# Performance work log

Measured on AMD Instinct MI355X. Metric: run time of the kernel, lower is better.

The kernel has to match this reference:

```python
import jax, jax.numpy as jnp
import numpy as np

N_NODES = 100000
N_EDGES = 1600000
D = 128
N_LAYERS = 3  # GIN num_layers = n_layers + 1 with n_layers = 2
BN_EPS = 1e-5


def _batchnorm(x, gamma, beta):
    # Training-mode BatchNorm1d over the node axis (biased variance, as torch uses
    # for normalization).
    mean = jnp.mean(x, axis=0)
    var = jnp.mean((x - mean) ** 2, axis=0)
    return (x - mean) * jax.lax.rsqrt(var + BN_EPS) * gamma + beta


def setup_inputs() -> dict:
    key = jax.random.key(0)
    ks = jax.random.split(key, 5)
    features = jax.random.normal(ks[0], (N_NODES, D), dtype=jnp.float32)
    W = jax.random.normal(ks[1], (N_LAYERS, D, D), dtype=jnp.float32) * 0.05
    b = jnp.zeros((N_LAYERS, D), dtype=jnp.float32)
    eps = jnp.zeros((N_LAYERS,), dtype=jnp.float32)  # learn_eps init 0
    bn1_gamma = jnp.ones((N_LAYERS, D), dtype=jnp.float32)
    bn1_beta = jnp.zeros((N_LAYERS, D), dtype=jnp.float32)
    bn2_gamma = jnp.ones((N_LAYERS, D), dtype=jnp.float32)
    bn2_beta = jnp.zeros((N_LAYERS, D), dtype=jnp.float32)
    src = jax.random.randint(ks[2], (N_EDGES,), 0, N_NODES, dtype=jnp.int64 if jax.config.jax_enable_x64 else jnp.int32)
    dst = jax.random.randint(ks[3], (N_EDGES,), 0, N_NODES, dtype=jnp.int64 if jax.config.jax_enable_x64 else jnp.int32)
    return {
        'features': features, 'W': W, 'b': b, 'eps': eps,
        'bn1_gamma': bn1_gamma, 'bn1_beta': bn1_beta,
        'bn2_gamma': bn2_gamma, 'bn2_beta': bn2_beta,
        'src': src, 'dst': dst,
    }


def reference(features, W, b, eps, bn1_gamma, bn1_beta, bn2_gamma, bn2_beta, src, dst):
    n = features.shape[0]
    h = features
    hidden_rep = [h]
    for i in range(N_LAYERS):
        # GINConv, 'sum' aggregation: (1+eps)*h_v + sum_{u->v} h_u
        agg = jax.ops.segment_sum(h[src], dst, num_segments=n)
        z = (1.0 + eps[i]) * h + agg
        # ApplyNodeFunc: Linear (num_mlp_layers=1) -> BN -> ReLU
        z = z @ W[i] + b[i]
        z = jax.nn.relu(_batchnorm(z, bn1_gamma[i], bn1_beta[i]))
        # GIN.forward: outer BN -> ReLU
        z = jax.nn.relu(_batchnorm(z, bn2_gamma[i], bn2_beta[i]))
        h = z
        hidden_rep.append(h)
    # torch.stack(hidden_rep) -> [n_layers+2, N, D]
    return jnp.stack(hidden_rep, axis=0)
```

## Files before the change

### kernel.cpp

```cpp
#include <hip/hip_runtime.h>
#include <hip/hip_bf16.h>

#define DD 128

typedef __attribute__((ext_vector_type(8))) short bfrag8;
typedef __attribute__((ext_vector_type(4))) float f32x4;

__device__ __forceinline__ float bf16lo(unsigned int u) {
    union { unsigned int i; float f; } c; c.i = u << 16; return c.f;
}
__device__ __forceinline__ float bf16hi(unsigned int u) {
    union { unsigned int i; float f; } c; c.i = u & 0xffff0000u; return c.f;
}
__device__ __forceinline__ unsigned short f2bf(float f) {
    union { float f; unsigned int i; } c; c.f = f;
    unsigned int x = c.i;
    unsigned int r = (x + 0x7fffu + ((x >> 16) & 1u)) >> 16;
    return (unsigned short)r;
}

__global__ void k_hist(const int* __restrict__ dst, int* __restrict__ deg, int E) {
    int i = blockIdx.x * blockDim.x + threadIdx.x;
    if (i < E) atomicAdd(&deg[dst[i]], 1);
}

__global__ void k_scan1(const int* __restrict__ deg, int* __restrict__ partials, int Nn) {
    __shared__ int s[1024];
    int i = blockIdx.x * 1024 + threadIdx.x;
    s[threadIdx.x] = (i < Nn) ? deg[i] : 0;
    __syncthreads();
    for (int off = 512; off > 0; off >>= 1) {
        if (threadIdx.x < off) s[threadIdx.x] += s[threadIdx.x + off];
        __syncthreads();
    }
    if (threadIdx.x == 0) partials[blockIdx.x] = s[0];
}

__global__ void k_scan2(const int* __restrict__ partials, int* __restrict__ pscan, int nb) {
    if (threadIdx.x == 0) {
        int acc = 0;
        for (int i = 0; i < nb; i++) { pscan[i] = acc; acc += partials[i]; }
    }
}

__global__ void k_scan3(const int* __restrict__ deg, const int* __restrict__ pscan,
                        int* __restrict__ row_start, int Nn, int E) {
    __shared__ int s[1024];
    int i = blockIdx.x * 1024 + threadIdx.x;
    int v = (i < Nn) ? deg[i] : 0;
    s[threadIdx.x] = v;
    __syncthreads();
    for (int off = 1; off < 1024; off <<= 1) {
        int t = (threadIdx.x >= off) ? s[threadIdx.x - off] : 0;
        __syncthreads();
        s[threadIdx.x] += t;
        __syncthreads();
    }
    if (i < Nn) row_start[i] = pscan[blockIdx.x] + s[threadIdx.x] - v;
    if (blockIdx.x == 0 && threadIdx.x == 0) row_start[Nn] = E;
}

__global__ void k_scatter(const int* __restrict__ src, const int* __restrict__ dst,
                          const int* __restrict__ row_start, int* __restrict__ cursor,
                          int* __restrict__ csr, int E) {
    int i = blockIdx.x * blockDim.x + threadIdx.x;
    if (i < E) {
        int d = dst[i];
        int pos = row_start[d] + atomicAdd(&cursor[d], 1);
        csr[pos] = src[i];
    }
}

__global__ void k_cvt_feat(const float* __restrict__ f, float* __restrict__ out0,
                           unsigned int* __restrict__ hb, int total4) {
    int i = blockIdx.x * blockDim.x + threadIdx.x;
    if (i >= total4) return;
    float4 v = ((const float4*)f)[i];
    ((float4*)out0)[i] = v;
    unsigned int lo = (unsigned int)f2bf(v.x) | ((unsigned int)f2bf(v.y) << 16);
    unsigned int hi = (unsigned int)f2bf(v.z) | ((unsigned int)f2bf(v.w) << 16);
    ((uint2*)hb)[i] = make_uint2(lo, hi);
}

__global__ void k_cvtW(const float* __restrict__ W, unsigned short* __restrict__ Wt, int total) {
    int i = blockIdx.x * blockDim.x + threadIdx.x;
    if (i >= total) return;
    int l = i >> 14;
    int r = i & 16383;
    int k = r >> 7, n = r & 127;
    Wt[(l << 14) + n * 128 + k] = f2bf(W[i]);
}

__global__ void k_gather(const unsigned int* __restrict__ hb, const int* __restrict__ row_start,
                         const int* __restrict__ csr, const float* __restrict__ eps, int layer,
                         unsigned int* __restrict__ zb, int Nn) {
    int wv = threadIdx.x >> 6, lane = threadIdx.x & 63;
    int v = blockIdx.x * 4 + wv;
    if (v >= Nn) return;
    float e1 = 1.0f + eps[layer];
    unsigned int hs = hb[v * 64 + lane];
    float ax = e1 * bf16lo(hs);
    float ay = e1 * bf16hi(hs);
    int beg = row_start[v], end = row_start[v + 1];
    int e = beg;
    for (; e + 3 < end; e += 4) {
        int u0 = csr[e], u1 = csr[e + 1], u2 = csr[e + 2], u3 = csr[e + 3];
        unsigned int h0 = hb[u0 * 64 + lane];
        unsigned int h1 = hb[u1 * 64 + lane];
        unsigned int h2 = hb[u2 * 64 + lane];
        unsigned int h3 = hb[u3 * 64 + lane];
        ax += bf16lo(h0) + bf16lo(h1) + bf16lo(h2) + bf16lo(h3);
        ay += bf16hi(h0) + bf16hi(h1) + bf16hi(h2) + bf16hi(h3);
    }
    for (; e < end; e++) {
        unsigned int hu = hb[csr[e] * 64 + lane];
        ax += bf16lo(hu); ay += bf16hi(hu);
    }
    zb[v * 64 + lane] = (unsigned int)f2bf(ax) | ((unsigned int)f2bf(ay) << 16);
}

__launch_bounds__(256)
__global__ void k_gemm(const unsigned short* __restrict__ zb, const unsigned short* __restrict__ Wt,
                       const float* __restrict__ bias, int layer, float* __restrict__ y,
                       float* __restrict__ s1sum, float* __restrict__ s1sq, int Nn) {
    __shared__ unsigned short Al[64 * 136];
    __shared__ unsigned short Bl[128 * 136];
    int tid = threadIdx.x;
    int m0 = blockIdx.x * 64;
    const unsigned short* Wl = Wt + (layer << 14);
    #pragma unroll
    for (int p = 0; p < 8; p++) {
        int slot = p * 256 + tid;
        int n = slot >> 4, c = slot & 15;
        *(uint4*)&Bl[n * 136 + c * 8] = *(const uint4*)&Wl[n * 128 + c * 8];
    }
    #pragma unroll
    for (int p = 0; p < 4; p++) {
        int slot = p * 256 + tid;
        int r = slot >> 4, c = slot & 15;
        int grow = m0 + r;
        uint4 val = make_uint4(0, 0, 0, 0);
        if (grow < Nn) val = *(const uint4*)&zb[(size_t)grow * 128 + c * 8];
        *(uint4*)&Al[r * 136 + c * 8] = val;
    }
    __syncthreads();

    int lane = tid & 63, wv = tid >> 6;
    int tcol = lane & 15, quad = lane >> 4;
    f32x4 acc[4][2];
    #pragma unroll
    for (int a = 0; a < 4; a++)
        #pragma unroll
        for (int b2 = 0; b2 < 2; b2++) acc[a][b2] = (f32x4){0.f, 0.f, 0.f, 0.f};

    #pragma unroll
    for (int kk = 0; kk < 128; kk += 32) {
        int kb = kk + quad * 8;
        bfrag8 af[4], bf[2];
        #pragma unroll
        for (int mt = 0; mt < 4; mt++)
            af[mt] = *(const bfrag8*)&Al[(16 * mt + tcol) * 136 + kb];
        #pragma unroll
        for (int nt = 0; nt < 2; nt++)
            bf[nt] = *(const bfrag8*)&Bl[(32 * wv + 16 * nt + tcol) * 136 + kb];
        #pragma unroll
        for (int mt = 0; mt < 4; mt++)
            #pragma unroll
            for (int nt = 0; nt < 2; nt++)
                acc[mt][nt] = __builtin_amdgcn_mfma_f32_16x16x32_bf16(af[mt], bf[nt], acc[mt][nt], 0, 0, 0);
    }

    #pragma unroll
    for (int nt = 0; nt < 2; nt++) {
        int col = 32 * wv + 16 * nt + tcol;
        float bcol = bias[layer * 128 + col];
        float psum = 0.f, psq = 0.f;
        #pragma unroll
        for (int mt = 0; mt < 4; mt++) {
            #pragma unroll
            for (int r = 0; r < 4; r++) {
                int row = m0 + 16 * mt + quad * 4 + r;
                float val = acc[mt][nt][r] + bcol;
                if (row < Nn) {
                    y[(size_t)row * 128 + col] = val;
                    psum += val;
                    psq += val * val;
                }
            }
        }
        psum += __shfl_xor(psum, 16); psq += __shfl_xor(psq, 16);
        psum += __shfl_xor(psum, 32); psq += __shfl_xor(psq, 32);
        if (lane < 16) {
            atomicAdd(&s1sum[col], psum);
            atomicAdd(&s1sq[col], psq);
        }
    }
}

__global__ void k_fin(float* __restrict__ sum, float* __restrict__ sq,
                      const float* __restrict__ gamma, const float* __restrict__ beta, int layer,
                      float* __restrict__ sc, float* __restrict__ sh, float invN) {
    int c = threadIdx.x;
    float m = sum[c] * invN;
    float var = sq[c] * invN - m * m;
    float rstd = rsqrtf(var + 1e-5f);
    float s = gamma[layer * 128 + c] * rstd;
    sc[c] = s;
    sh[c] = beta[layer * 128 + c] - m * s;
    sum[c] = 0.f;
    sq[c] = 0.f;
}

__global__ void k_stats2(const float* __restrict__ y, const float* __restrict__ s1,
                         const float* __restrict__ sh1, float* __restrict__ s2sum,
                         float* __restrict__ s2sq, int Nn) {
    int c = threadIdx.x & 127;
    int r0 = blockIdx.x * 2 + (threadIdx.x >> 7);
    float sc = s1[c], sh = sh1[c];
    float sum = 0.f, sq = 0.f;
    int stride = gridDim.x * 2;
    for (int r = r0; r < Nn; r += stride) {
        float t = fmaxf(y[(size_t)r * 128 + c] * sc + sh, 0.f);
        sum += t;
        sq += t * t;
    }
    atomicAdd(&s2sum[c], sum);
    atomicAdd(&s2sq[c], sq);
}

__global__ void k_apply(float* __restrict__ y, const float* __restrict__ s1,
                        const float* __restrict__ sh1, const float* __restrict__ s2,
                        const float* __restrict__ sh2, unsigned int* __restrict__ hb, int total4) {
    int i = blockIdx.x * blockDim.x + threadIdx.x;
    if (i >= total4) return;
    int c = (i * 4) & 127;
    float4 v = ((float4*)y)[i];
    float t0 = fmaxf(v.x * s1[c] + sh1[c], 0.f);
    float t1 = fmaxf(v.y * s1[c + 1] + sh1[c + 1], 0.f);
    float t2 = fmaxf(v.z * s1[c + 2] + sh1[c + 2], 0.f);
    float t3 = fmaxf(v.w * s1[c + 3] + sh1[c + 3], 0.f);
    float o0 = fmaxf(t0 * s2[c] + sh2[c], 0.f);
    float o1 = fmaxf(t1 * s2[c + 1] + sh2[c + 1], 0.f);
    float o2 = fmaxf(t2 * s2[c + 2] + sh2[c + 2], 0.f);
    float o3 = fmaxf(t3 * s2[c + 3] + sh2[c + 3], 0.f);
    ((float4*)y)[i] = make_float4(o0, o1, o2, o3);
    unsigned int lo = (unsigned int)f2bf(o0) | ((unsigned int)f2bf(o1) << 16);
    unsigned int hi = (unsigned int)f2bf(o2) | ((unsigned int)f2bf(o3) << 16);
    ((uint2*)hb)[i] = make_uint2(lo, hi);
}

extern "C" void kernel_launch(void* const* d_in, const int* in_sizes, int n_in,
                              void* d_out, int out_size, void* d_ws, size_t ws_size,
                              hipStream_t stream) {
    const float* features = (const float*)d_in[0];
    const float* W        = (const float*)d_in[1];
    const float* bias     = (const float*)d_in[2];
    const float* eps      = (const float*)d_in[3];
    const float* g1       = (const float*)d_in[4];
    const float* b1       = (const float*)d_in[5];
    const float* g2       = (const float*)d_in[6];
    const float* b2       = (const float*)d_in[7];
    const int*   src      = (const int*)d_in[8];
    const int*   dst      = (const int*)d_in[9];

    const int Nn = in_sizes[0] / DD;
    const int E  = in_sizes[8];
    const int L  = 3;
    float* out = (float*)d_out;

    char* w = (char*)d_ws;
    auto alloc = [&](size_t bytes) -> char* {
        char* p = w;
        w += (bytes + 255) & ~(size_t)255;
        return p;
    };
    int* deg       = (int*)alloc((size_t)Nn * 4);
    int* cursor    = (int*)alloc((size_t)Nn * 4);
    int* row_start = (int*)alloc((size_t)(Nn + 1) * 4);
    int* partials  = (int*)alloc(1024);
    int* pscan     = (int*)alloc(1024);
    int* csr       = (int*)alloc((size_t)E * 4);
    unsigned int* hb = (unsigned int*)alloc((size_t)Nn * 64 * 4);
    unsigned int* zb = (unsigned int*)alloc((size_t)Nn * 64 * 4);
    unsigned short* Wt = (unsigned short*)alloc((size_t)3 * 128 * 128 * 2);
    float* s1sum = (float*)alloc(512);
    float* s1sq  = (float*)alloc(512);
    float* s2sum = (float*)alloc(512);
    float* s2sq  = (float*)alloc(512);
    float* s1    = (float*)alloc(512);
    float* sh1   = (float*)alloc(512);
    float* s2    = (float*)alloc(512);
    float* sh2   = (float*)alloc(512);

    hipMemsetAsync(deg, 0, (size_t)Nn * 4, stream);
    hipMemsetAsync(cursor, 0, (size_t)Nn * 4, stream);
    hipMemsetAsync(s1sum, 0, 4 * 512, stream);

    const int nb = (Nn + 1023) / 1024;
    k_hist<<<(E + 255) / 256, 256, 0, stream>>>(dst, deg, E);
    k_scan1<<<nb, 1024, 0, stream>>>(deg, partials, Nn);
    k_scan2<<<1, 64, 0, stream>>>(partials, pscan, nb);
    k_scan3<<<nb, 1024, 0, stream>>>(deg, pscan, row_start, Nn, E);
    k_scatter<<<(E + 255) / 256, 256, 0, stream>>>(src, dst, row_start, cursor, csr, E);

    const int total4 = Nn * DD / 4;
    k_cvt_feat<<<(total4 + 255) / 256, 256, 0, stream>>>(features, out, hb, total4);
    k_cvtW<<<(3 * 128 * 128 + 255) / 256, 256, 0, stream>>>(W, Wt, 3 * 128 * 128);

    const float invN = 1.0f / (float)Nn;
    for (int l = 0; l < L; l++) {
        float* y = out + (size_t)(l + 1) * Nn * DD;
        k_gather<<<(Nn + 3) / 4, 256, 0, stream>>>(hb, row_start, csr, eps, l, zb, Nn);
        k_gemm<<<(Nn + 63) / 64, 256, 0, stream>>>((const unsigned short*)zb, Wt, bias, l, y,
                                                   s1sum, s1sq, Nn);
        k_fin<<<1, 128, 0, stream>>>(s1sum, s1sq, g1, b1, l, s1, sh1, invN);
        k_stats2<<<512, 256, 0, stream>>>(y, s1, sh1, s2sum, s2sq, Nn);
        k_fin<<<1, 128, 0, stream>>>(s2sum, s2sq, g2, b2, l, s2, sh2, invN);
        k_apply<<<(total4 + 255) / 256, 256, 0, stream>>>(y, s1, sh1, s2, sh2, hb, total4);
    }
}
```

Measured before the change: 991.3 us.

## Fuse setup kernels, fold BN finalize into stats/apply, unroll gather by eight

Merges histogram, feature conversion and weight conversion into one grid-stride setup kernel, and collapses the three-kernel scan into two with vectorised 4-per-thread loads. The BN finalize kernels are removed: stats2 and apply now compute scale and shift in shared memory, and stats2 reduces per block before doing global atomics. The gather loop is unrolled to eight neighbours for more loads in flight. The GEMM now writes to a scratch buffer instead of the output, and per-layer stats buffers are zeroed by a single memset. This cuts launch count and global atomic traffic, at the cost of redundant per-block finalize work and extra workspace memory.

```diff
diff --git a/kernel.cpp b/kernel.cpp
--- a/kernel.cpp
+++ b/kernel.cpp
@@ -19,45 +19,88 @@
     return (unsigned short)r;
 }
 
-__global__ void k_hist(const int* __restrict__ dst, int* __restrict__ deg, int E) {
-    int i = blockIdx.x * blockDim.x + threadIdx.x;
-    if (i < E) atomicAdd(&deg[dst[i]], 1);
+__global__ void k_setup(const int* __restrict__ dst, int* __restrict__ deg, int E,
+                        const float* __restrict__ features, float* __restrict__ out0,
+                        unsigned int* __restrict__ hb, int total4,
+                        const float* __restrict__ W, unsigned short* __restrict__ Wt) {
+    int gtid = blockIdx.x * blockDim.x + threadIdx.x;
+    int gsz = gridDim.x * blockDim.x;
+    for (int i = gtid; i < E; i += gsz) atomicAdd(&deg[dst[i]], 1);
+    for (int i = gtid; i < total4; i += gsz) {
+        float4 v = ((const float4*)features)[i];
+        ((float4*)out0)[i] = v;
+        unsigned int lo = (unsigned int)f2bf(v.x) | ((unsigned int)f2bf(v.y) << 16);
+        unsigned int hi = (unsigned int)f2bf(v.z) | ((unsigned int)f2bf(v.w) << 16);
+        ((uint2*)hb)[i] = make_uint2(lo, hi);
+    }
+    for (int i = gtid; i < 3 * 128 * 128; i += gsz) {
+        int l = i >> 14, r = i & 16383, k = r >> 7, n = r & 127;
+        Wt[(l << 14) + n * 128 + k] = f2bf(W[i]);
+    }
 }
 
 __global__ void k_scan1(const int* __restrict__ deg, int* __restrict__ partials, int Nn) {
-    __shared__ int s[1024];
-    int i = blockIdx.x * 1024 + threadIdx.x;
-    s[threadIdx.x] = (i < Nn) ? deg[i] : 0;
-    __syncthreads();
-    for (int off = 512; off > 0; off >>= 1) {
-        if (threadIdx.x < off) s[threadIdx.x] += s[threadIdx.x + off];
-        __syncthreads();
-    }
-    if (threadIdx.x == 0) partials[blockIdx.x] = s[0];
-}
-
-__global__ void k_scan2(const int* __restrict__ partials, int* __restrict__ pscan, int nb) {
-    if (threadIdx.x == 0) {
-        int acc = 0;
-        for (int i = 0; i < nb; i++) { pscan[i] = acc; acc += partials[i]; }
-    }
-}
-
-__global__ void k_scan3(const int* __restrict__ deg, const int* __restrict__ pscan,
-                        int* __restrict__ row_start, int Nn, int E) {
-    __shared__ int s[1024];
-    int i = blockIdx.x * 1024 + threadIdx.x;
-    int v = (i < Nn) ? deg[i] : 0;
-    s[threadIdx.x] = v;
-    __syncthreads();
-    for (int off = 1; off < 1024; off <<= 1) {
-        int t = (threadIdx.x >= off) ? s[threadIdx.x - off] : 0;
-        __syncthreads();
-        s[threadIdx.x] += t;
-        __syncthreads();
-    }
-    if (i < Nn) row_start[i] = pscan[blockIdx.x] + s[threadIdx.x] - v;
-    if (blockIdx.x == 0 && threadIdx.x == 0) row_start[Nn] = E;
+    __shared__ int sm[256];
+    int tid = threadIdx.x;
+    int base = (blockIdx.x << 10) + 4 * tid;
+    int s = 0;
+    if (base + 3 < Nn) {
+        int4 v = *(const int4*)&deg[base];
+        s = v.x + v.y + v.z + v.w;
+    } else {
+        for (int j = 0; j < 4; j++) if (base + j < Nn) s += deg[base + j];
+    }
+    sm[tid] = s;
+    __syncthreads();
+    for (int off = 128; off > 0; off >>= 1) {
+        if (tid < off) sm[tid] += sm[tid + off];
+        __syncthreads();
+    }
+    if (tid == 0) partials[blockIdx.x] = sm[0];
+}
+
+__global__ void k_scan3(const int* __restrict__ deg, const int* __restrict__ partials,
+                        int* __restrict__ row_start, int Nn, int E, int nchunk) {
+    __shared__ int sp[256];
+    __shared__ int sm[256];
+    int tid = threadIdx.x, c = blockIdx.x;
+    int p = (tid < nchunk) ? partials[tid] : 0;
+    sp[tid] = p;
+    __syncthreads();
+    for (int off = 1; off < 256; off <<= 1) {
+        int t = (tid >= off) ? sp[tid - off] : 0;
+        __syncthreads();
+        sp[tid] += t;
+        __syncthreads();
+    }
+    int chunkpref = (c == 0) ? 0 : sp[c - 1];
+
+    int base = (c << 10) + 4 * tid;
+    int d0 = 0, d1 = 0, d2 = 0, d3 = 0;
+    if (base + 3 < Nn) {
+        int4 v = *(const int4*)&deg[base];
+        d0 = v.x; d1 = v.y; d2 = v.z; d3 = v.w;
+    } else {
+        if (base + 0 < Nn) d0 = deg[base + 0];
+        if (base + 1 < Nn) d1 = deg[base + 1];
+        if (base + 2 < Nn) d2 = deg[base + 2];
+        if (base + 3 < Nn) d3 = deg[base + 3];
+    }
+    int ts = d0 + d1 + d2 + d3;
+    sm[tid] = ts;
+    __syncthreads();
+    for (int off = 1; off < 256; off <<= 1) {
+        int t = (tid >= off) ? sm[tid - off] : 0;
+        __syncthreads();
+        sm[tid] += t;
+        __syncthreads();
+    }
+    int run = chunkpref + sm[tid] - ts;
+    if (base + 0 < Nn) row_start[base + 0] = run; run += d0;
+    if (base + 1 < Nn) row_start[base + 1] = run; run += d1;
+    if (base + 2 < Nn) row_start[base + 2] = run; run += d2;
+    if (base + 3 < Nn) row_start[base + 3] = run;
+    if (c == 0 && tid == 0) row_start[Nn] = E;
 }
 
 __global__ void k_scatter(const int* __restrict__ src, const int* __restrict__ dst,
@@ -71,26 +114,6 @@
     }
 }
 
-__global__ void k_cvt_feat(const float* __restrict__ f, float* __restrict__ out0,
-                           unsigned int* __restrict__ hb, int total4) {
-    int i = blockIdx.x * blockDim.x + threadIdx.x;
-    if (i >= total4) return;
-    float4 v = ((const float4*)f)[i];
-    ((float4*)out0)[i] = v;
-    unsigned int lo = (unsigned int)f2bf(v.x) | ((unsigned int)f2bf(v.y) << 16);
-    unsigned int hi = (unsigned int)f2bf(v.z) | ((unsigned int)f2bf(v.w) << 16);
-    ((uint2*)hb)[i] = make_uint2(lo, hi);
-}
-
-__global__ void k_cvtW(const float* __restrict__ W, unsigned short* __restrict__ Wt, int total) {
-    int i = blockIdx.x * blockDim.x + threadIdx.x;
-    if (i >= total) return;
-    int l = i >> 14;
-    int r = i & 16383;
-    int k = r >> 7, n = r & 127;
-    Wt[(l << 14) + n * 128 + k] = f2bf(W[i]);
-}
-
 __global__ void k_gather(const unsigned int* __restrict__ hb, const int* __restrict__ row_start,
                          const int* __restrict__ csr, const float* __restrict__ eps, int layer,
                          unsigned int* __restrict__ zb, int Nn) {
@@ -98,31 +121,38 @@
     int v = blockIdx.x * 4 + wv;
     if (v >= Nn) return;
     float e1 = 1.0f + eps[layer];
-    unsigned int hs = hb[v * 64 + lane];
+    unsigned int hs = hb[(size_t)v * 64 + lane];
     float ax = e1 * bf16lo(hs);
     float ay = e1 * bf16hi(hs);
     int beg = row_start[v], end = row_start[v + 1];
     int e = beg;
-    for (; e + 3 < end; e += 4) {
+    for (; e + 7 < end; e += 8) {
         int u0 = csr[e], u1 = csr[e + 1], u2 = csr[e + 2], u3 = csr[e + 3];
-        unsigned int h0 = hb[u0 * 64 + lane];
-        unsigned int h1 = hb[u1 * 64 + lane];
-        unsigned int h2 = hb[u2 * 64 + lane];
-        unsigned int h3 = hb[u3 * 64 + lane];
-        ax += bf16lo(h0) + bf16lo(h1) + bf16lo(h2) + bf16lo(h3);
-        ay += bf16hi(h0) + bf16hi(h1) + bf16hi(h2) + bf16hi(h3);
+        int u4 = csr[e + 4], u5 = csr[e + 5], u6 = csr[e + 6], u7 = csr[e + 7];
+        unsigned int h0 = hb[(size_t)u0 * 64 + lane];
+        unsigned int h1 = hb[(size_t)u1 * 64 + lane];
+        unsigned int h2 = hb[(size_t)u2 * 64 + lane];
+        unsigned int h3 = hb[(size_t)u3 * 64 + lane];
+        unsigned int h4 = hb[(size_t)u4 * 64 + lane];
+        unsigned int h5 = hb[(size_t)u5 * 64 + lane];
+        unsigned int h6 = hb[(size_t)u6 * 64 + lane];
+        unsigned int h7 = hb[(size_t)u7 * 64 + lane];
+        ax += bf16lo(h0) + bf16lo(h1) + bf16lo(h2) + bf16lo(h3)
+            + bf16lo(h4) + bf16lo(h5) + bf16lo(h6) + bf16lo(h7);
+        ay += bf16hi(h0) + bf16hi(h1) + bf16hi(h2) + bf16hi(h3)
+            + bf16hi(h4) + bf16hi(h5) + bf16hi(h6) + bf16hi(h7);
     }
     for (; e < end; e++) {
-        unsigned int hu = hb[csr[e] * 64 + lane];
+        unsigned int hu = hb[(size_t)csr[e] * 64 + lane];
         ax += bf16lo(hu); ay += bf16hi(hu);
     }
-    zb[v * 64 + lane] = (unsigned int)f2bf(ax) | ((unsigned int)f2bf(ay) << 16);
+    zb[(size_t)v * 64 + lane] = (unsigned int)f2bf(ax) | ((unsigned int)f2bf(ay) << 16);
 }
 
 __launch_bounds__(256)
 __global__ void k_gemm(const unsigned short* __restrict__ zb, const unsigned short* __restrict__ Wt,
                        const float* __restrict__ bias, int layer, float* __restrict__ y,
-                       float* __restrict__ s1sum, float* __restrict__ s1sq, int Nn) {
+                       float* __restrict__ stl, int Nn) {
     __shared__ unsigned short Al[64 * 136];
     __shared__ unsigned short Bl[128 * 136];
     int tid = threadIdx.x;
@@ -191,62 +221,114 @@
         psum += __shfl_xor(psum, 16); psq += __shfl_xor(psq, 16);
         psum += __shfl_xor(psum, 32); psq += __shfl_xor(psq, 32);
         if (lane < 16) {
-            atomicAdd(&s1sum[col], psum);
-            atomicAdd(&s1sq[col], psq);
+            atomicAdd(&stl[col], psum);
+            atomicAdd(&stl[128 + col], psq);
         }
     }
 }
 
-__global__ void k_fin(float* __restrict__ sum, float* __restrict__ sq,
-                      const float* __restrict__ gamma, const float* __restrict__ beta, int layer,
-                      float* __restrict__ sc, float* __restrict__ sh, float invN) {
-    int c = threadIdx.x;
-    float m = sum[c] * invN;
-    float var = sq[c] * invN - m * m;
-    float rstd = rsqrtf(var + 1e-5f);
-    float s = gamma[layer * 128 + c] * rstd;
-    sc[c] = s;
-    sh[c] = beta[layer * 128 + c] - m * s;
-    sum[c] = 0.f;
-    sq[c] = 0.f;
-}
-
-__global__ void k_stats2(const float* __restrict__ y, const float* __restrict__ s1,
-                         const float* __restrict__ sh1, float* __restrict__ s2sum,
-                         float* __restrict__ s2sq, int Nn) {
-    int c = threadIdx.x & 127;
-    int r0 = blockIdx.x * 2 + (threadIdx.x >> 7);
-    float sc = s1[c], sh = sh1[c];
-    float sum = 0.f, sq = 0.f;
-    int stride = gridDim.x * 2;
-    for (int r = r0; r < Nn; r += stride) {
-        float t = fmaxf(y[(size_t)r * 128 + c] * sc + sh, 0.f);
-        sum += t;
-        sq += t * t;
-    }
-    atomicAdd(&s2sum[c], sum);
-    atomicAdd(&s2sq[c], sq);
-}
-
-__global__ void k_apply(float* __restrict__ y, const float* __restrict__ s1,
-                        const float* __restrict__ sh1, const float* __restrict__ s2,
-                        const float* __restrict__ sh2, unsigned int* __restrict__ hb, int total4) {
-    int i = blockIdx.x * blockDim.x + threadIdx.x;
-    if (i >= total4) return;
-    int c = (i * 4) & 127;
-    float4 v = ((float4*)y)[i];
-    float t0 = fmaxf(v.x * s1[c] + sh1[c], 0.f);
-    float t1 = fmaxf(v.y * s1[c + 1] + sh1[c + 1], 0.f);
-    float t2 = fmaxf(v.z * s1[c + 2] + sh1[c + 2], 0.f);
-    float t3 = fmaxf(v.w * s1[c + 3] + sh1[c + 3], 0.f);
-    float o0 = fmaxf(t0 * s2[c] + sh2[c], 0.f);
-    float o1 = fmaxf(t1 * s2[c + 1] + sh2[c + 1], 0.f);
-    float o2 = fmaxf(t2 * s2[c + 2] + sh2[c + 2], 0.f);
-    float o3 = fmaxf(t3 * s2[c + 3] + sh2[c + 3], 0.f);
-    ((float4*)y)[i] = make_float4(o0, o1, o2, o3);
-    unsigned int lo = (unsigned int)f2bf(o0) | ((unsigned int)f2bf(o1) << 16);
-    unsigned int hi = (unsigned int)f2bf(o2) | ((unsigned int)f2bf(o3) << 16);
-    ((uint2*)hb)[i] = make_uint2(lo, hi);
+__launch_bounds__(256)
+__global__ void k_stats2(const float* __restrict__ y, float* __restrict__ stl,
+                         const float* __restrict__ g1, const float* __restrict__ b1,
+                         int layer, int total4, float invN) {
+    __shared__ float red[512];
+    int tid = threadIdx.x;
+    if (tid < 128) {
+        float m = stl[tid] * invN;
+        float var = stl[128 + tid] * invN - m * m;
+        float rstd = rsqrtf(var + 1e-5f);
+        float s = g1[layer * 128 + tid] * rstd;
+        red[tid] = s;
+        red[128 + tid] = b1[layer * 128 + tid] - m * s;
+        red[256 + tid] = 0.f;
+        red[384 + tid] = 0.f;
+    }
+    __syncthreads();
+    int lane = tid & 63;
+    int cbase = (4 * tid) & 127;
+    float s1r[4], sh1r[4];
+    #pragma unroll
+    for (int j = 0; j < 4; j++) { s1r[j] = red[cbase + j]; sh1r[j] = red[128 + cbase + j]; }
+    float ps[4] = {0.f, 0.f, 0.f, 0.f}, pq[4] = {0.f, 0.f, 0.f, 0.f};
+    int gtid = blockIdx.x * 256 + tid;
+    int gsz = gridDim.x * 256;
+    for (int i = gtid; i < total4; i += gsz) {
+        float4 v = ((const float4*)y)[i];
+        float t0 = fmaxf(v.x * s1r[0] + sh1r[0], 0.f);
+        float t1 = fmaxf(v.y * s1r[1] + sh1r[1], 0.f);
+        float t2 = fmaxf(v.z * s1r[2] + sh1r[2], 0.f);
+        float t3 = fmaxf(v.w * s1r[3] + sh1r[3], 0.f);
+        ps[0] += t0; pq[0] += t0 * t0;
+        ps[1] += t1; pq[1] += t1 * t1;
+        ps[2] += t2; pq[2] += t2 * t2;
+        ps[3] += t3; pq[3] += t3 * t3;
+    }
+    #pragma unroll
+    for (int j = 0; j < 4; j++) {
+        ps[j] += __shfl_xor(ps[j], 32);
+        pq[j] += __shfl_xor(pq[j], 32);
+    }
+    if (lane < 32) {
+        #pragma unroll
+        for (int j = 0; j < 4; j++) {
+            atomicAdd(&red[256 + cbase + j], ps[j]);
+            atomicAdd(&red[384 + cbase + j], pq[j]);
+        }
+    }
+    __syncthreads();
+    if (tid < 128) {
+        atomicAdd(&stl[256 + tid], red[256 + tid]);
+        atomicAdd(&stl[384 + tid], red[384 + tid]);
+    }
+}
+
+__launch_bounds__(256)
+__global__ void k_apply(const float* __restrict__ y, const float* __restrict__ stl,
+                        const float* __restrict__ g1, const float* __restrict__ b1,
+                        const float* __restrict__ g2, const float* __restrict__ b2,
+                        int layer, float* __restrict__ outl, unsigned int* __restrict__ hb,
+                        int total4, float invN) {
+    __shared__ float red[512];
+    int tid = threadIdx.x;
+    if (tid < 128) {
+        float m1 = stl[tid] * invN;
+        float v1 = stl[128 + tid] * invN - m1 * m1;
+        float r1 = rsqrtf(v1 + 1e-5f);
+        float s1 = g1[layer * 128 + tid] * r1;
+        red[tid] = s1;
+        red[128 + tid] = b1[layer * 128 + tid] - m1 * s1;
+        float m2 = stl[256 + tid] * invN;
+        float v2 = stl[384 + tid] * invN - m2 * m2;
+        float r2 = rsqrtf(v2 + 1e-5f);
+        float s2 = g2[layer * 128 + tid] * r2;
+        red[256 + tid] = s2;
+        red[384 + tid] = b2[layer * 128 + tid] - m2 * s2;
+    }
+    __syncthreads();
+    int cbase = (4 * tid) & 127;
+    float s1a[4], sh1a[4], s2a[4], sh2a[4];
+    #pragma unroll
+    for (int j = 0; j < 4; j++) {
+        s1a[j]  = red[cbase + j];       sh1a[j] = red[128 + cbase + j];
+        s2a[j]  = red[256 + cbase + j]; sh2a[j] = red[384 + cbase + j];
+    }
+    int gtid = blockIdx.x * 256 + tid;
+    int gsz = gridDim.x * 256;
+    for (int i = gtid; i < total4; i += gsz) {
+        float4 v = ((const float4*)y)[i];
+        float t0 = fmaxf(v.x * s1a[0] + sh1a[0], 0.f);
+        float t1 = fmaxf(v.y * s1a[1] + sh1a[1], 0.f);
+        float t2 = fmaxf(v.z * s1a[2] + sh1a[2], 0.f);
+        float t3 = fmaxf(v.w * s1a[3] + sh1a[3], 0.f);
+        float o0 = fmaxf(t0 * s2a[0] + sh2a[0], 0.f);
+        float o1 = fmaxf(t1 * s2a[1] + sh2a[1], 0.f);
+        float o2 = fmaxf(t2 * s2a[2] + sh2a[2], 0.f);
+        float o3 = fmaxf(t3 * s2a[3] + sh2a[3], 0.f);
+        ((float4*)outl)[i] = make_float4(o0, o1, o2, o3);
+        unsigned int lo = (unsigned int)f2bf(o0) | ((unsigned int)f2bf(o1) << 16);
+        unsigned int hi = (unsigned int)f2bf(o2) | ((unsigned int)f2bf(o3) << 16);
+        ((uint2*)hb)[i] = make_uint2(lo, hi);
+    }
 }
 
 extern "C" void kernel_launch(void* const* d_in, const int* in_sizes, int n_in,
@@ -265,7 +347,6 @@
 
     const int Nn = in_sizes[0] / DD;
     const int E  = in_sizes[8];
-    const int L  = 3;
     float* out = (float*)d_out;
 
     char* w = (char*)d_ws;
@@ -274,48 +355,36 @@
         w += (bytes + 255) & ~(size_t)255;
         return p;
     };
-    int* deg       = (int*)alloc((size_t)Nn * 4);
-    int* cursor    = (int*)alloc((size_t)Nn * 4);
+    int*   deg    = (int*)alloc((size_t)Nn * 4);
+    int*   cursor = (int*)alloc((size_t)Nn * 4);
+    float* stats  = (float*)alloc(3 * 512 * 4);
+    char*  zero_end = w;
     int* row_start = (int*)alloc((size_t)(Nn + 1) * 4);
     int* partials  = (int*)alloc(1024);
-    int* pscan     = (int*)alloc(1024);
     int* csr       = (int*)alloc((size_t)E * 4);
     unsigned int* hb = (unsigned int*)alloc((size_t)Nn * 64 * 4);
     unsigned int* zb = (unsigned int*)alloc((size_t)Nn * 64 * 4);
     unsigned short* Wt = (unsigned short*)alloc((size_t)3 * 128 * 128 * 2);
-    float* s1sum = (float*)alloc(512);
-    float* s1sq  = (float*)alloc(512);
-    float* s2sum = (float*)alloc(512);
-    float* s2sq  = (float*)alloc(512);
-    float* s1    = (float*)alloc(512);
-    float* sh1   = (float*)alloc(512);
-    float* s2    = (float*)alloc(512);
-    float* sh2   = (float*)alloc(512);
-
-    hipMemsetAsync(deg, 0, (size_t)Nn * 4, stream);
-    hipMemsetAsync(cursor, 0, (size_t)Nn * 4, stream);
-    hipMemsetAsync(s1sum, 0, 4 * 512, stream);
-
-    const int nb = (Nn + 1023) / 1024;
-    k_hist<<<(E + 255) / 256, 256, 0, stream>>>(dst, deg, E);
-    k_scan1<<<nb, 1024, 0, stream>>>(deg, partials, Nn);
-    k_scan2<<<1, 64, 0, stream>>>(partials, pscan, nb);
-    k_scan3<<<nb, 1024, 0, stream>>>(deg, pscan, row_start, Nn, E);
+    float* yb = (float*)alloc((size_t)Nn * 128 * 4);
+
+    const int total4 = Nn * DD / 4;
+    const float invN = 1.0f / (float)Nn;
+    const int nchunk = (Nn + 1023) / 1024;
+
+    hipMemsetAsync(deg, 0, (size_t)(zero_end - (char*)deg), stream);
+
+    k_setup<<<(E + 255) / 256, 256, 0, stream>>>(dst, deg, E, features, out, hb, total4, W, Wt);
+    k_scan1<<<nchunk, 256, 0, stream>>>(deg, partials, Nn);
+    k_scan3<<<nchunk, 256, 0, stream>>>(deg, partials, row_start, Nn, E, nchunk);
     k_scatter<<<(E + 255) / 256, 256, 0, stream>>>(src, dst, row_start, cursor, csr, E);
 
-    const int total4 = Nn * DD / 4;
-    k_cvt_feat<<<(total4 + 255) / 256, 256, 0, stream>>>(features, out, hb, total4);
-    k_cvtW<<<(3 * 128 * 128 + 255) / 256, 256, 0, stream>>>(W, Wt, 3 * 128 * 128);
-
-    const float invN = 1.0f / (float)Nn;
-    for (int l = 0; l < L; l++) {
-        float* y = out + (size_t)(l + 1) * Nn * DD;
+    for (int l = 0; l < 3; l++) {
+        float* stl = stats + l * 512;
+        float* outl = out + (size_t)(l + 1) * Nn * DD;
         k_gather<<<(Nn + 3) / 4, 256, 0, stream>>>(hb, row_start, csr, eps, l, zb, Nn);
-        k_gemm<<<(Nn + 63) / 64, 256, 0, stream>>>((const unsigned short*)zb, Wt, bias, l, y,
-                                                   s1sum, s1sq, Nn);
-        k_fin<<<1, 128, 0, stream>>>(s1sum, s1sq, g1, b1, l, s1, sh1, invN);
-        k_stats2<<<512, 256, 0, stream>>>(y, s1, sh1, s2sum, s2sq, Nn);
-        k_fin<<<1, 128, 0, stream>>>(s2sum, s2sq, g2, b2, l, s2, sh2, invN);
-        k_apply<<<(total4 + 255) / 256, 256, 0, stream>>>(y, s1, sh1, s2, sh2, hb, total4);
-    }
-}
+        k_gemm<<<(Nn + 63) / 64, 256, 0, stream>>>((const unsigned short*)zb, Wt, bias, l, yb,
+                                                   stl, Nn);
+        k_stats2<<<512, 256, 0, stream>>>(yb, stl, g1, b1, l, total4, invN);
+        k_apply<<<1024, 256, 0, stream>>>(yb, stl, g1, b1, g2, b2, l, outl, hb, total4, invN);
+    }
+}
```

New measurement: 865.5 us. 1.15x faster.
